# Performance work log

Measured on AMD Instinct MI355X. Metric: run time of the kernel, lower is better.

Reference implementation:

```python
import jax, jax.numpy as jnp
import numpy as np

TOTAL = 819200   # total flattened labels
BATCH = 16384    # number of samples (segments)
DIM = 128        # embed_dim
LABELS_PER = 50  # constant segment length (TOTAL = BATCH * LABELS_PER)


def setup_inputs() -> dict:
    key = jax.random.key(0)
    k_emb, k_w1, k_b1, k_w2, k_b2 = jax.random.split(key, 5)
    embeddings = jax.random.normal(k_emb, (TOTAL, DIM), dtype=jnp.float32)
    # weight_net params (PyTorch nn.Linear default-ish init scale)
    s1 = 1.0 / np.sqrt(DIM)
    W1 = jax.random.uniform(k_w1, (DIM, DIM), jnp.float32, -s1, s1)
    b1 = jax.random.uniform(k_b1, (DIM,), jnp.float32, -s1, s1)
    W2 = jax.random.uniform(k_w2, (DIM, 1), jnp.float32, -s1, s1)
    b2 = jax.random.uniform(k_b2, (1,), jnp.float32, -s1, s1)
    lengths = jnp.full((BATCH,), LABELS_PER, dtype=jnp.int32)
    return {"embeddings": embeddings, "W1": W1, "b1": b1, "W2": W2, "b2": b2,
            "lengths": lengths}


def reference(embeddings, W1, b1, W2, b2, lengths):
    # MLP scorer: Linear -> ReLU -> Linear -> Softmax(dim=0) (GLOBAL over all labels)
    h = jnp.maximum(embeddings @ W1 + b1, 0.0)           # (T, D)
    scores = h @ W2 + b2                                  # (T, 1)
    weights = jax.nn.softmax(scores, axis=0)              # (T, 1) global softmax
    # Ragged per-segment weighted sum via segment_sum
    batch = lengths.shape[0]
    total = embeddings.shape[0]
    seg_ids = jnp.repeat(jnp.arange(batch, dtype=jnp.int32), lengths,
                         total_repeat_length=total)       # (T,)
    pooled = jax.ops.segment_sum(embeddings * weights, seg_ids,
                                 num_segments=batch)      # (B, D)
    return pooled
```

## Files before the change

### kernel.cpp

```cpp
#include <hip/hip_runtime.h>
#include <hip/hip_bf16.h>
#include <math.h>

#define DIM 128

typedef __attribute__((ext_vector_type(8))) short bf16x8;
typedef __attribute__((ext_vector_type(4))) float f32x4;

union FragU { bf16x8 v; __hip_bfloat162 h[4]; };

static __device__ __forceinline__ ushort f2bf(float f) {
    unsigned u = __float_as_uint(f);
    u += 0x7FFFu + ((u >> 16) & 1u);
    return (ushort)(u >> 16);
}

typedef __attribute__((address_space(1))) const unsigned GASp;
typedef __attribute__((address_space(3))) unsigned LASp;
static __device__ __forceinline__ void gll16(const void* g, void* l) {
    __builtin_amdgcn_global_load_lds((GASp*)g, (LASp*)l, 16, 0, 0);
}

static __device__ __forceinline__ void stage16(float* buf, const float* emb,
                                               long row0, long Tm1, int lane) {
    #pragma unroll
    for (int i = 0; i < 8; ++i) {
        int s = i * 64 + lane;
        int r = s >> 5, x = s & 31;
        long gr = row0 + r; gr = (gr > Tm1) ? Tm1 : gr;
        gll16(emb + gr * 128 + ((x ^ (r & 7)) << 2), (char*)buf + i * 1024);
    }
}

__global__ __launch_bounds__(1024) void scan_kernel(const int* __restrict__ lengths,
                                                    int* __restrict__ offsets, int batch) {
    __shared__ int tsum[1024];
    int tid = threadIdx.x;
    int per = (batch + 1023) >> 10;
    int start = tid * per;
    int s = 0;
    for (int i = 0; i < per; ++i) {
        int idx = start + i;
        if (idx < batch) s += lengths[idx];
    }
    tsum[tid] = s;
    __syncthreads();
    for (int off = 1; off < 1024; off <<= 1) {
        int v = (tid >= off) ? tsum[tid - off] : 0;
        __syncthreads();
        tsum[tid] += v;
        __syncthreads();
    }
    int base = (tid == 0) ? 0 : tsum[tid - 1];
    for (int i = 0; i < per; ++i) {
        int idx = start + i;
        if (idx < batch) { offsets[idx] = base; base += lengths[idx]; }
    }
}

__global__ __launch_bounds__(256, 2) void fused_kernel(
        const float* __restrict__ emb, const float* __restrict__ W1,
        const float* __restrict__ b1, const float* __restrict__ W2,
        const float* __restrict__ b2, const int* __restrict__ offsets,
        const int* __restrict__ lengths, int batch, int T,
        float* __restrict__ mArr, float* __restrict__ sArr,
        float* __restrict__ tvec) {
    __shared__ __align__(16) char smem[65536];

    int tid = threadIdx.x;
    int lane = tid & 63;
    int wv = tid >> 6;
    int lr = lane & 15;
    int lg = lane >> 4;

    ushort* sB = (ushort*)smem;
    for (int i = 0; i < 16; ++i) {
        int q = tid + i * 256;
        int n = q >> 5;
        int k4 = q & 31;
        ushort4 w;
        w.x = f2bf(W1[(k4 * 4 + 0) * DIM + n]);
        w.y = f2bf(W1[(k4 * 4 + 1) * DIM + n]);
        w.z = f2bf(W1[(k4 * 4 + 2) * DIM + n]);
        w.w = f2bf(W1[(k4 * 4 + 3) * DIM + n]);
        int c = k4 >> 1;
        int a16 = n * 128 + ((c ^ (n & 7)) * 8) + (k4 & 1) * 4;
        *(ushort4*)&sB[a16] = w;
    }
    __syncthreads();
    bf16x8 bfrag[8][4];
    #pragma unroll
    for (int ct = 0; ct < 8; ++ct) {
        int n = ct * 16 + lr;
        #pragma unroll
        for (int kc = 0; kc < 4; ++kc) {
            int c = lg + kc * 4;
            bfrag[ct][kc] = *(const bf16x8*)&sB[n * 128 + ((c ^ (n & 7)) * 8)];
        }
    }
    float b1reg[8], w2reg[8];
    #pragma unroll
    for (int ct = 0; ct < 8; ++ct) {
        b1reg[ct] = b1[ct * 16 + lr];
        w2reg[ct] = W2[ct * 16 + lr];
    }
    float b2v = b2[0];
    __syncthreads();

    float* buf0 = (float*)(smem + wv * 16384);
    float* buf1 = (float*)(smem + wv * 16384 + 8192);

    long Tm1 = (long)T - 1;
    int nwaves = gridDim.x * 4;
    int gwave = blockIdx.x * 4 + wv;
    int per = (batch + nwaves - 1) / nwaves;
    int seg0 = gwave * per;
    int seg1 = seg0 + per; if (seg1 > batch) seg1 = batch;

    for (int seg = seg0; seg < seg1; ++seg) {
        long off = offsets[seg];
        int len = lengths[seg];
        int nch = (len + 15) >> 4;
        float m_run = -INFINITY, S_run = 0.f, t0 = 0.f, t1 = 0.f;

        if (nch > 0) stage16(buf0, emb, off, Tm1, lane);
        if (nch > 1) stage16(buf1, emb, off + 16, Tm1, lane);

        for (int c = 0; c < nch; ++c) {
            float* bufc = (c & 1) ? buf1 : buf0;
            if (c + 1 < nch) asm volatile("s_waitcnt vmcnt(8)" ::: "memory");
            else             asm volatile("s_waitcnt vmcnt(0)" ::: "memory");

            bf16x8 a[4];
            #pragma unroll
            for (int kc = 0; kc < 4; ++kc) {
                int c0 = kc * 8 + lg * 2;
                float4 q0 = *(const float4*)&bufc[(lr * 32 + (c0 ^ (lr & 7))) * 4];
                float4 q1 = *(const float4*)&bufc[(lr * 32 + ((c0 + 1) ^ (lr & 7))) * 4];
                FragU f;
                f.h[0] = __float22bfloat162_rn(make_float2(q0.x, q0.y));
                f.h[1] = __float22bfloat162_rn(make_float2(q0.z, q0.w));
                f.h[2] = __float22bfloat162_rn(make_float2(q1.x, q1.y));
                f.h[3] = __float22bfloat162_rn(make_float2(q1.z, q1.w));
                a[kc] = f.v;
            }

            f32x4 acc[8];
            #pragma unroll
            for (int ct = 0; ct < 8; ++ct) acc[ct] = (f32x4)(0.f);
            #pragma unroll
            for (int ct = 0; ct < 8; ++ct)
                #pragma unroll
                for (int kc = 0; kc < 4; ++kc)
                    acc[ct] = __builtin_amdgcn_mfma_f32_16x16x32_bf16(a[kc], bfrag[ct][kc], acc[ct], 0, 0, 0);

            float p[4];
            #pragma unroll
            for (int reg = 0; reg < 4; ++reg) {
                float s = 0.f;
                #pragma unroll
                for (int ct = 0; ct < 8; ++ct) {
                    float h = acc[ct][reg] + b1reg[ct];
                    h = fmaxf(h, 0.f);
                    s = fmaf(h, w2reg[ct], s);
                }
                p[reg] = s;
            }
            #pragma unroll
            for (int m = 1; m < 16; m <<= 1) {
                #pragma unroll
                for (int reg = 0; reg < 4; ++reg)
                    p[reg] += __shfl_xor(p[reg], m, 64);
            }
            int r3 = lane & 3;
            float pr = p[0];
            pr = (r3 == 1) ? p[1] : pr;
            pr = (r3 == 2) ? p[2] : pr;
            pr = (r3 == 3) ? p[3] : pr;
            int src = ((lane & 12) << 2) + r3;
            float sv = __shfl(pr, src, 64);

            int cv = len - c * 16;
            float s_l = (lr < cv) ? (sv + b2v) : -INFINITY;
            float m_c = s_l;
            #pragma unroll
            for (int o = 1; o < 16; o <<= 1) m_c = fmaxf(m_c, __shfl_xor(m_c, o, 64));
            float m_new = fmaxf(m_run, m_c);
            float ea = expf(m_run - m_new);
            float w_l = expf(s_l - m_new);
            float S_c = w_l;
            #pragma unroll
            for (int o = 1; o < 16; o <<= 1) S_c += __shfl_xor(S_c, o, 64);
            S_run = S_run * ea + S_c;
            m_run = m_new;

            t0 *= ea; t1 *= ea;
            int xc = lane >> 1, xh = lane & 1;
            #pragma unroll
            for (int j = 0; j < 16; ++j) {
                float wj = __uint_as_float(__builtin_amdgcn_readlane(__float_as_uint(w_l), j));
                float2 e = *(const float2*)&bufc[(j * 32 + (xc ^ (j & 7))) * 4 + xh * 2];
                t0 = fmaf(wj, e.x, t0);
                t1 = fmaf(wj, e.y, t1);
            }

            asm volatile("s_waitcnt lgkmcnt(0)" ::: "memory");
            if (c + 2 < nch) stage16(bufc, emb, off + (long)(c + 2) * 16, Tm1, lane);
        }

        *(float2*)&tvec[(long)seg * DIM + 2 * lane] = make_float2(t0, t1);
        if (lane == 0) { mArr[seg] = m_run; sArr[seg] = S_run; }
    }
}

__global__ __launch_bounds__(1024) void segreduce_kernel(const float* __restrict__ mArr,
        const float* __restrict__ sArr, int batch, float* __restrict__ stats) {
    __shared__ float redm[16], reds[16];
    int tid = threadIdx.x;
    int wave = tid >> 6, ln = tid & 63;
    float m = -INFINITY;
    for (int i = tid; i < batch; i += 1024) m = fmaxf(m, mArr[i]);
    #pragma unroll
    for (int o = 32; o >= 1; o >>= 1) m = fmaxf(m, __shfl_xor(m, o, 64));
    if (ln == 0) redm[wave] = m;
    __syncthreads();
    float M = -INFINITY;
    #pragma unroll
    for (int k = 0; k < 16; ++k) M = fmaxf(M, redm[k]);
    float s = 0.f;
    for (int i = tid; i < batch; i += 1024) s += sArr[i] * expf(mArr[i] - M);
    #pragma unroll
    for (int o = 32; o >= 1; o >>= 1) s += __shfl_xor(s, o, 64);
    if (ln == 0) reds[wave] = s;
    __syncthreads();
    if (tid == 0) {
        float S = 0.f;
        #pragma unroll
        for (int k = 0; k < 16; ++k) S += reds[k];
        stats[0] = M;
        stats[1] = 1.0f / S;
    }
}

__global__ __launch_bounds__(256) void scale_kernel(const float* __restrict__ tvec,
        const float* __restrict__ mArr, const float* __restrict__ stats,
        float* __restrict__ out, int n) {
    int idx = blockIdx.x * 256 + threadIdx.x;
    if (idx >= n) return;
    float M = stats[0], invS = stats[1];
    int b = idx >> 7;
    out[idx] = tvec[idx] * (expf(mArr[b] - M) * invS);
}

extern "C" void kernel_launch(void* const* d_in, const int* in_sizes, int n_in,
                              void* d_out, int out_size, void* d_ws, size_t ws_size,
                              hipStream_t stream) {
    const float* emb     = (const float*)d_in[0];
    const float* W1      = (const float*)d_in[1];
    const float* b1      = (const float*)d_in[2];
    const float* W2      = (const float*)d_in[3];
    const float* b2      = (const float*)d_in[4];
    const int*   lengths = (const int*)d_in[5];
    int T = in_sizes[0] / DIM;
    int batch = in_sizes[5];
    float* out = (float*)d_out;

    int*   offsets = (int*)d_ws;
    float* mArr    = (float*)(offsets + batch);
    float* sArr    = mArr + batch;
    float* stats   = sArr + batch;
    float* tvec    = stats + 2;

    scan_kernel<<<1, 1024, 0, stream>>>(lengths, offsets, batch);
    fused_kernel<<<512, 256, 0, stream>>>(emb, W1, b1, W2, b2, offsets, lengths,
                                          batch, T, mArr, sArr, tvec);
    segreduce_kernel<<<1, 1024, 0, stream>>>(mArr, sArr, batch, stats);
    scale_kernel<<<(out_size + 255) / 256, 256, 0, stream>>>(tvec, mArr, stats, out, out_size);
}
```

Before: 166.1 us.

## Stream contiguous row range per wave instead of per-segment 16-row chunks

Each wave now treats its assigned segments as one contiguous run of rows and processes them in dense 16-row chunks, splitting softmax/accumulation state at segment boundaries inside a chunk. With 50-row segments, the old per-segment loop wasted part of each last chunk (64 rows loaded and run through the MFMA for 50 valid) and restarted the double-buffer pipeline at every segment. The new path removes that padding and keeps prefetch running across segments. In exchange it adds a variable inner loop with extra reductions and exps wherever a chunk spans two segments.

```diff
diff --git a/kernel.cpp b/kernel.cpp
--- a/kernel.cpp
+++ b/kernel.cpp
@@ -114,17 +114,19 @@
     int nwaves = gridDim.x * 4;
     int gwave = blockIdx.x * 4 + wv;
     int per = (batch + nwaves - 1) / nwaves;
-    int seg0 = gwave * per;
-    int seg1 = seg0 + per; if (seg1 > batch) seg1 = batch;
-
-    for (int seg = seg0; seg < seg1; ++seg) {
-        long off = offsets[seg];
-        int len = lengths[seg];
-        int nch = (len + 15) >> 4;
+    int seg = gwave * per;
+    int segend = seg + per; if (segend > batch) segend = batch;
+
+    if (seg < segend) {
+        long row0 = offsets[seg];
+        long rowend = (segend < batch) ? (long)offsets[segend] : (long)T;
+        int nch = (int)((rowend - row0 + 15) >> 4);
+        int rows_left = lengths[seg];
         float m_run = -INFINITY, S_run = 0.f, t0 = 0.f, t1 = 0.f;
-
-        if (nch > 0) stage16(buf0, emb, off, Tm1, lane);
-        if (nch > 1) stage16(buf1, emb, off + 16, Tm1, lane);
+        int xc = lane >> 1, xh = lane & 1;
+
+        if (nch > 0) stage16(buf0, emb, row0, Tm1, lane);
+        if (nch > 1) stage16(buf1, emb, row0 + 16, Tm1, lane);
 
         for (int c = 0; c < nch; ++c) {
             float* bufc = (c & 1) ? buf1 : buf0;
@@ -178,38 +180,62 @@
             pr = (r3 == 2) ? p[2] : pr;
             pr = (r3 == 3) ? p[3] : pr;
             int src = ((lane & 12) << 2) + r3;
-            float sv = __shfl(pr, src, 64);
-
-            int cv = len - c * 16;
-            float s_l = (lr < cv) ? (sv + b2v) : -INFINITY;
-            float m_c = s_l;
-            #pragma unroll
-            for (int o = 1; o < 16; o <<= 1) m_c = fmaxf(m_c, __shfl_xor(m_c, o, 64));
-            float m_new = fmaxf(m_run, m_c);
-            float ea = expf(m_run - m_new);
-            float w_l = expf(s_l - m_new);
-            float S_c = w_l;
-            #pragma unroll
-            for (int o = 1; o < 16; o <<= 1) S_c += __shfl_xor(S_c, o, 64);
-            S_run = S_run * ea + S_c;
-            m_run = m_new;
-
-            t0 *= ea; t1 *= ea;
-            int xc = lane >> 1, xh = lane & 1;
-            #pragma unroll
-            for (int j = 0; j < 16; ++j) {
-                float wj = __uint_as_float(__builtin_amdgcn_readlane(__float_as_uint(w_l), j));
-                float2 e = *(const float2*)&bufc[(j * 32 + (xc ^ (j & 7))) * 4 + xh * 2];
-                t0 = fmaf(wj, e.x, t0);
-                t1 = fmaf(wj, e.y, t1);
+            float sv = __shfl(pr, src, 64) + b2v;
+
+            int vrows = (int)(rowend - row0 - (long)c * 16);
+            if (vrows > 16) vrows = 16;
+            int pos = 0;
+            while (pos < vrows) {
+                int take = vrows - pos;
+                if (take > rows_left) take = rows_left;
+                int end = pos + take;
+                bool val = (lr >= pos) && (lr < end);
+                float s_l = val ? sv : -INFINITY;
+                float m_c = s_l;
+                #pragma unroll
+                for (int o = 1; o < 16; o <<= 1) m_c = fmaxf(m_c, __shfl_xor(m_c, o, 64));
+                float m_new = fmaxf(m_run, m_c);
+                float ea = expf(m_run - m_new);
+                float w_l = expf(s_l - m_new);
+                float S_c = w_l;
+                #pragma unroll
+                for (int o = 1; o < 16; o <<= 1) S_c += __shfl_xor(S_c, o, 64);
+                S_run = S_run * ea + S_c;
+                m_run = m_new;
+                t0 *= ea; t1 *= ea;
+
+                if (pos == 0 && end == 16) {
+                    #pragma unroll
+                    for (int j = 0; j < 16; ++j) {
+                        float wj = __uint_as_float(__builtin_amdgcn_readlane(__float_as_uint(w_l), j));
+                        float2 e = *(const float2*)&bufc[(j * 32 + (xc ^ (j & 7))) * 4 + xh * 2];
+                        t0 = fmaf(wj, e.x, t0);
+                        t1 = fmaf(wj, e.y, t1);
+                    }
+                } else {
+                    for (int j = pos; j < end; ++j) {
+                        float wj = __uint_as_float(__builtin_amdgcn_readlane(__float_as_uint(w_l), j));
+                        float2 e = *(const float2*)&bufc[(j * 32 + (xc ^ (j & 7))) * 4 + xh * 2];
+                        t0 = fmaf(wj, e.x, t0);
+                        t1 = fmaf(wj, e.y, t1);
+                    }
+                }
+
+                rows_left -= take;
+                pos = end;
+                if (rows_left == 0) {
+                    *(float2*)&tvec[(long)seg * DIM + 2 * lane] = make_float2(t0, t1);
+                    if (lane == 0) { mArr[seg] = m_run; sArr[seg] = S_run; }
+                    m_run = -INFINITY; S_run = 0.f; t0 = 0.f; t1 = 0.f;
+                    ++seg;
+                    if (seg >= segend) break;
+                    rows_left = lengths[seg];
+                }
             }
 
             asm volatile("s_waitcnt lgkmcnt(0)" ::: "memory");
-            if (c + 2 < nch) stage16(bufc, emb, off + (long)(c + 2) * 16, Tm1, lane);
+            if (c + 2 < nch) stage16(bufc, emb, row0 + (long)(c + 2) * 16, Tm1, lane);
         }
-
-        *(float2*)&tvec[(long)seg * DIM + 2 * lane] = make_float2(t0, t1);
-        if (lane == 0) { mArr[seg] = m_run; sArr[seg] = S_run; }
     }
 }
 
```

After: 180.5 us. 8.7% more time.

## Prefetch across segment boundaries and use lazy online-softmax rescaling

Applied to the files above, without the earlier changes.

Staging of the double-buffered chunk pipeline now continues across segment boundaries, so the first chunks of the next segment load while the current one finishes and the per-segment pipeline drain goes away. The online softmax only rescales when some score exceeds the running reference by more than 8, drops b2 (it cancels in the global softmax), switches to __expf, and defers the per-lane sum reduction to segment end. This removes per-chunk max and sum shuffles and exp calls, at the cost of a larger dynamic range in the accumulators and slightly less accurate exponentials. Any downstream use of b2 in the combine kernel must stay consistent.

```diff
diff --git a/kernel.cpp b/kernel.cpp
--- a/kernel.cpp
+++ b/kernel.cpp
@@ -104,7 +104,6 @@
         b1reg[ct] = b1[ct * 16 + lr];
         w2reg[ct] = W2[ct * 16 + lr];
     }
-    float b2v = b2[0];
     __syncthreads();
 
     float* buf0 = (float*)(smem + wv * 16384);
@@ -115,101 +114,127 @@
     int gwave = blockIdx.x * 4 + wv;
     int per = (batch + nwaves - 1) / nwaves;
     int seg0 = gwave * per;
-    int seg1 = seg0 + per; if (seg1 > batch) seg1 = batch;
-
-    for (int seg = seg0; seg < seg1; ++seg) {
-        long off = offsets[seg];
-        int len = lengths[seg];
-        int nch = (len + 15) >> 4;
-        float m_run = -INFINITY, S_run = 0.f, t0 = 0.f, t1 = 0.f;
-
-        if (nch > 0) stage16(buf0, emb, off, Tm1, lane);
-        if (nch > 1) stage16(buf1, emb, off + 16, Tm1, lane);
-
-        for (int c = 0; c < nch; ++c) {
-            float* bufc = (c & 1) ? buf1 : buf0;
-            if (c + 1 < nch) asm volatile("s_waitcnt vmcnt(8)" ::: "memory");
-            else             asm volatile("s_waitcnt vmcnt(0)" ::: "memory");
-
-            bf16x8 a[4];
+    int segend = seg0 + per; if (segend > batch) segend = batch;
+
+    if (seg0 < segend) {
+        int xc = lane >> 1, xh = lane & 1;
+
+        int ss = seg0, sc = 0;
+        long soff = offsets[ss];
+        int snch = (lengths[ss] + 15) >> 4;
+        int staged = 0, consumed = 0;
+
+        #pragma unroll
+        for (int k = 0; k < 2; ++k) {
+            if (ss < segend) {
+                stage16((staged & 1) ? buf1 : buf0, emb, soff + (long)sc * 16, Tm1, lane);
+                ++staged;
+                if (++sc == snch) {
+                    sc = 0; ++ss;
+                    if (ss < segend) { soff = offsets[ss]; snch = (lengths[ss] + 15) >> 4; }
+                }
+            }
+        }
+
+        for (int seg = seg0; seg < segend; ++seg) {
+            int len = lengths[seg];
+            int nch = (len + 15) >> 4;
+            float r_ref = -INFINITY, Sp = 0.f, t0 = 0.f, t1 = 0.f;
+
+            for (int c = 0; c < nch; ++c) {
+                float* bufc = (consumed & 1) ? buf1 : buf0;
+                if (staged - consumed >= 2) asm volatile("s_waitcnt vmcnt(8)" ::: "memory");
+                else                        asm volatile("s_waitcnt vmcnt(0)" ::: "memory");
+                ++consumed;
+
+                bf16x8 a[4];
+                #pragma unroll
+                for (int kc = 0; kc < 4; ++kc) {
+                    int c0 = kc * 8 + lg * 2;
+                    float4 q0 = *(const float4*)&bufc[(lr * 32 + (c0 ^ (lr & 7))) * 4];
+                    float4 q1 = *(const float4*)&bufc[(lr * 32 + ((c0 + 1) ^ (lr & 7))) * 4];
+                    FragU f;
+                    f.h[0] = __float22bfloat162_rn(make_float2(q0.x, q0.y));
+                    f.h[1] = __float22bfloat162_rn(make_float2(q0.z, q0.w));
+                    f.h[2] = __float22bfloat162_rn(make_float2(q1.x, q1.y));
+                    f.h[3] = __float22bfloat162_rn(make_float2(q1.z, q1.w));
+                    a[kc] = f.v;
+                }
+
+                f32x4 acc[8];
+                #pragma unroll
+                for (int ct = 0; ct < 8; ++ct) acc[ct] = (f32x4)(0.f);
+                #pragma unroll
+                for (int ct = 0; ct < 8; ++ct)
+                    #pragma unroll
+                    for (int kc = 0; kc < 4; ++kc)
+                        acc[ct] = __builtin_amdgcn_mfma_f32_16x16x32_bf16(a[kc], bfrag[ct][kc], acc[ct], 0, 0, 0);
+
+                float p[4];
+                #pragma unroll
+                for (int reg = 0; reg < 4; ++reg) {
+                    float s = 0.f;
+                    #pragma unroll
+                    for (int ct = 0; ct < 8; ++ct) {
+                        float h = acc[ct][reg] + b1reg[ct];
+                        h = fmaxf(h, 0.f);
+                        s = fmaf(h, w2reg[ct], s);
+                    }
+                    p[reg] = s;
+                }
+                #pragma unroll
+                for (int m = 1; m < 16; m <<= 1) {
+                    #pragma unroll
+                    for (int reg = 0; reg < 4; ++reg)
+                        p[reg] += __shfl_xor(p[reg], m, 64);
+                }
+                int r3 = lane & 3;
+                float pr = p[0];
+                pr = (r3 == 1) ? p[1] : pr;
+                pr = (r3 == 2) ? p[2] : pr;
+                pr = (r3 == 3) ? p[3] : pr;
+                int src = ((lane & 12) << 2) + r3;
+                float sv = __shfl(pr, src, 64);
+
+                int cv = len - c * 16;
+                float s_l = (lr < cv) ? sv : -INFINITY;
+
+                if (!__all(s_l - r_ref <= 8.f)) {
+                    float m_c = s_l;
+                    #pragma unroll
+                    for (int o = 1; o < 16; o <<= 1) m_c = fmaxf(m_c, __shfl_xor(m_c, o, 64));
+                    float r_new = fmaxf(r_ref, m_c);
+                    float scale = __expf(r_ref - r_new);
+                    Sp *= scale; t0 *= scale; t1 *= scale;
+                    r_ref = r_new;
+                }
+                float w_l = __expf(s_l - r_ref);
+                Sp += w_l;
+
+                #pragma unroll
+                for (int j = 0; j < 16; ++j) {
+                    float wj = __uint_as_float(__builtin_amdgcn_readlane(__float_as_uint(w_l), j));
+                    float2 e = *(const float2*)&bufc[(j * 32 + (xc ^ (j & 7))) * 4 + xh * 2];
+                    t0 = fmaf(wj, e.x, t0);
+                    t1 = fmaf(wj, e.y, t1);
+                }
+
+                asm volatile("s_waitcnt lgkmcnt(0)" ::: "memory");
+                if (ss < segend) {
+                    stage16((staged & 1) ? buf1 : buf0, emb, soff + (long)sc * 16, Tm1, lane);
+                    ++staged;
+                    if (++sc == snch) {
+                        sc = 0; ++ss;
+                        if (ss < segend) { soff = offsets[ss]; snch = (lengths[ss] + 15) >> 4; }
+                    }
+                }
+            }
+
             #pragma unroll
-            for (int kc = 0; kc < 4; ++kc) {
-                int c0 = kc * 8 + lg * 2;
-                float4 q0 = *(const float4*)&bufc[(lr * 32 + (c0 ^ (lr & 7))) * 4];
-                float4 q1 = *(const float4*)&bufc[(lr * 32 + ((c0 + 1) ^ (lr & 7))) * 4];
-                FragU f;
-                f.h[0] = __float22bfloat162_rn(make_float2(q0.x, q0.y));
-                f.h[1] = __float22bfloat162_rn(make_float2(q0.z, q0.w));
-                f.h[2] = __float22bfloat162_rn(make_float2(q1.x, q1.y));
-                f.h[3] = __float22bfloat162_rn(make_float2(q1.z, q1.w));
-                a[kc] = f.v;
-            }
-
-            f32x4 acc[8];
-            #pragma unroll
-            for (int ct = 0; ct < 8; ++ct) acc[ct] = (f32x4)(0.f);
-            #pragma unroll
-            for (int ct = 0; ct < 8; ++ct)
-                #pragma unroll
-                for (int kc = 0; kc < 4; ++kc)
-                    acc[ct] = __builtin_amdgcn_mfma_f32_16x16x32_bf16(a[kc], bfrag[ct][kc], acc[ct], 0, 0, 0);
-
-            float p[4];
-            #pragma unroll
-            for (int reg = 0; reg < 4; ++reg) {
-                float s = 0.f;
-                #pragma unroll
-                for (int ct = 0; ct < 8; ++ct) {
-                    float h = acc[ct][reg] + b1reg[ct];
-                    h = fmaxf(h, 0.f);
-                    s = fmaf(h, w2reg[ct], s);
-                }
-                p[reg] = s;
-            }
-            #pragma unroll
-            for (int m = 1; m < 16; m <<= 1) {
-                #pragma unroll
-                for (int reg = 0; reg < 4; ++reg)
-                    p[reg] += __shfl_xor(p[reg], m, 64);
-            }
-            int r3 = lane & 3;
-            float pr = p[0];
-            pr = (r3 == 1) ? p[1] : pr;
-            pr = (r3 == 2) ? p[2] : pr;
-            pr = (r3 == 3) ? p[3] : pr;
-            int src = ((lane & 12) << 2) + r3;
-            float sv = __shfl(pr, src, 64);
-
-            int cv = len - c * 16;
-            float s_l = (lr < cv) ? (sv + b2v) : -INFINITY;
-            float m_c = s_l;
-            #pragma unroll
-            for (int o = 1; o < 16; o <<= 1) m_c = fmaxf(m_c, __shfl_xor(m_c, o, 64));
-            float m_new = fmaxf(m_run, m_c);
-            float ea = expf(m_run - m_new);
-            float w_l = expf(s_l - m_new);
-            float S_c = w_l;
-            #pragma unroll
-            for (int o = 1; o < 16; o <<= 1) S_c += __shfl_xor(S_c, o, 64);
-            S_run = S_run * ea + S_c;
-            m_run = m_new;
-
-            t0 *= ea; t1 *= ea;
-            int xc = lane >> 1, xh = lane & 1;
-            #pragma unroll
-            for (int j = 0; j < 16; ++j) {
-                float wj = __uint_as_float(__builtin_amdgcn_readlane(__float_as_uint(w_l), j));
-                float2 e = *(const float2*)&bufc[(j * 32 + (xc ^ (j & 7))) * 4 + xh * 2];
-                t0 = fmaf(wj, e.x, t0);
-                t1 = fmaf(wj, e.y, t1);
-            }
-
-            asm volatile("s_waitcnt lgkmcnt(0)" ::: "memory");
-            if (c + 2 < nch) stage16(bufc, emb, off + (long)(c + 2) * 16, Tm1, lane);
+            for (int o = 1; o < 16; o <<= 1) Sp += __shfl_xor(Sp, o, 64);
+            *(float2*)&tvec[(long)seg * DIM + 2 * lane] = make_float2(t0, t1);
+            if (lane == 0) { mArr[seg] = r_ref; sArr[seg] = Sp; }
         }
-
-        *(float2*)&tvec[(long)seg * DIM + 2 * lane] = make_float2(t0, t1);
-        if (lane == 0) { mArr[seg] = m_run; sArr[seg] = S_run; }
     }
 }
 
```

Result: slower. 229.7 us (+38.3%).
